# Kernel tuning notes

Measured on AMD Instinct MI355X. Metric: run time of the kernel, lower is better.

## Reference

```python
import jax, jax.numpy as jnp
import numpy as np

# LDPC-like Tanner graph: N variable nodes, M check nodes, dv edges per variable
N_VAR = 8192
N_CHK = 4096
DV = 3
N_EDGE = N_VAR * DV  # 24576 = code.H.E
BATCH = 128
T = 30               # opt.T iterations
EPS = 1e-7


def setup_inputs() -> dict:
    key = jax.random.key(0)
    k1, k2 = jax.random.split(key)
    # channel LLRs for a batch of received codewords, shape (N_VAR, BATCH)
    chn_llr = jax.random.normal(k1, (N_VAR, BATCH), dtype=jnp.float32) * 2.0
    # Tanner graph edge lists: edge e connects variable edge_var[e] <-> check edge_chk[e]
    edge_var = jnp.repeat(jnp.arange(N_VAR, dtype=jnp.int32), DV)
    edge_chk = jax.random.randint(k2, (N_EDGE,), 0, N_CHK, dtype=jnp.int32)
    # gamma_logit = 0  ->  sigmoid = 0.5 = damping_init
    gamma_logit = jnp.zeros((1,), dtype=jnp.float32)
    return {"chn_llr": chn_llr, "gamma_logit": gamma_logit,
            "edge_var": edge_var, "edge_chk": edge_chk}


def reference(chn_llr, gamma_logit, edge_var, edge_chk):
    """T damped sum-product BP iterations over the Tanner graph.

    Returns stacked per-iteration posterior LLRs, shape (T, N_VAR, BATCH).
    """
    gamma = jax.nn.sigmoid(gamma_logit[0])  # damping gate, shared (tie=True)
    segsum = jax.ops.segment_sum

    def step(carry, _):
        msg_C2V, msg_V2C = carry  # each (N_EDGE, BATCH)
        # ---- variable -> check update (extrinsic sum), damped by gamma ----
        var_sum = segsum(msg_C2V, edge_var, num_segments=N_VAR)        # (N_VAR, B)
        v2c_new = chn_llr[edge_var] + var_sum[edge_var] - msg_C2V       # (E, B)
        msg_V2C = gamma * v2c_new + (1.0 - gamma) * msg_V2C
        # ---- check -> variable update (tanh product rule, log/sign domain) ----
        t = jnp.tanh(jnp.clip(msg_V2C, -15.0, 15.0) * 0.5)              # (E, B)
        logabs = jnp.log(jnp.maximum(jnp.abs(t), EPS))
        neg = (t < 0.0).astype(msg_V2C.dtype)
        chk_log = segsum(logabs, edge_chk, num_segments=N_CHK)          # (N_CHK, B)
        chk_neg = segsum(neg, edge_chk, num_segments=N_CHK)
        ext_log = chk_log[edge_chk] - logabs                            # exclude self
        ext_sign = 1.0 - 2.0 * jnp.mod(chk_neg[edge_chk] - neg, 2.0)
        prod = jnp.clip(ext_sign * jnp.exp(ext_log), -1.0 + EPS, 1.0 - EPS)
        msg_C2V = 2.0 * jnp.arctanh(prod)
        # ---- per-iteration posterior LLR output ----
        out = chn_llr + segsum(msg_C2V, edge_var, num_segments=N_VAR)   # (N_VAR, B)
        return (msg_C2V, msg_V2C), out

    init = (jnp.zeros((N_EDGE, BATCH), dtype=chn_llr.dtype),
            jnp.zeros((N_EDGE, BATCH), dtype=chn_llr.dtype))
    _, outputs = jax.lax.scan(step, init, None, length=T)
    return outputs  # (T, N_VAR, BATCH)
```

## Files before the change

kernel.cpp:

```cpp
#include <hip/hip_runtime.h>
#include <math.h>

#define N_VAR 8192
#define N_CHK 4096
#define DV 3
#define N_EDGE (N_VAR * DV)
#define BATCH 128
#define T_ITERS 30
#define ELLW 24
#define SLOT_MAX (N_EDGE + 3 * N_CHK)

#define LOG2E 1.44269504088896340736f
#define LN2   0.69314718055994530942f

typedef _Float16 h4 __attribute__((ext_vector_type(4)));
typedef _Float16 h2 __attribute__((ext_vector_type(2)));

__device__ __forceinline__ float tanh_half(float x) {
    float ex = __builtin_amdgcn_exp2f(x * LOG2E);
    float t = 1.0f - 2.0f * __builtin_amdgcn_rcpf(ex + 1.0f);
    float s = (x < 0.0f) ? -1.0f : 1.0f;
    return s * fmaxf(fabsf(t), 1e-7f);
}

__device__ __forceinline__ float atanh2(float p) {
    const float lim = 1.0f - 1e-7f;
    p = fminf(fmaxf(p, -lim), lim);
    return (__builtin_amdgcn_logf(1.0f + p) -
            __builtin_amdgcn_logf(1.0f - p)) * LN2;
}

__device__ __forceinline__ float rcp_nr(float x) {
    float r = __builtin_amdgcn_rcpf(x);
    return r * (2.0f - x * r);
}


__global__ void k_ell_scatter(const int* __restrict__ edge_chk,
                              int* __restrict__ deg_arr, int* __restrict__ ell_e) {
    int e = blockIdx.x * blockDim.x + threadIdx.x;
    if (e < N_EDGE) {
        int c = edge_chk[e];
        int pos = atomicAdd(&deg_arr[c], 1);
        if (pos < ELLW) ell_e[c * ELLW + pos] = e;
    }
}

__global__ void k_hist(const int* __restrict__ deg_arr, int* __restrict__ hist) {
    int c = blockIdx.x * 256 + threadIdx.x;
    if (c < N_CHK) {
        int d = deg_arr[c]; if (d > ELLW) d = ELLW;
        atomicAdd(&hist[d], 1);
    }
}

__global__ void k_buckets(const int* __restrict__ hist,
                          int* __restrict__ bucket_base,
                          int* __restrict__ slot_off) {
    if (threadIdx.x == 0 && blockIdx.x == 0) {
        int cb = 0, sb = 0;
        for (int d = 0; d <= ELLW; ++d) {
            bucket_base[d] = cb;
            slot_off[d] = sb;
            int pd = (d == 0) ? 0 : ((d + 3) & ~3);
            cb += hist[d];
            sb += hist[d] * pd;
        }
    }
}

__global__ void k_place(const int* __restrict__ deg_arr, int* __restrict__ cursor,
                        const int* __restrict__ bucket_base,
                        const int* __restrict__ slot_off,
                        int* __restrict__ s_desc_g, int* __restrict__ chk_base) {
    int c = blockIdx.x * 256 + threadIdx.x;
    if (c < N_CHK) {
        int d = deg_arr[c]; if (d > ELLW) d = ELLW;
        int pd = (d + 3) & ~3;
        int pos = atomicAdd(&cursor[d], 1);
        int i = bucket_base[d] + pos;
        int base = slot_off[d] + pos * pd;
        s_desc_g[i] = (base << 5) | d;
        chk_base[c] = base;
    }
}

__global__ void k_slotmap2(const int* __restrict__ ell_e,
                           const int* __restrict__ deg_arr,
                           const int* __restrict__ chk_base,
                           int* __restrict__ slot_e) {
    int gid = blockIdx.x * 256 + threadIdx.x;
    if (gid < N_CHK * ELLW) {
        int c = gid / ELLW;
        int j = gid - c * ELLW;
        int d = deg_arr[c]; if (d > ELLW) d = ELLW;
        if (j < d) slot_e[ell_e[gid]] = chk_base[c] + j;
    }
}

__global__ void k_slot4(const int* __restrict__ slot_e, int4* __restrict__ slot4) {
    int v = blockIdx.x * 256 + threadIdx.x;
    if (v < N_VAR) {
        int4 s;
        s.x = slot_e[3 * v + 0];
        s.y = slot_e[3 * v + 1];
        s.z = slot_e[3 * v + 2];
        s.w = 0;
        slot4[v] = s;
    }
}


__global__ __launch_bounds__(1024) void k_bp2(
        const float* __restrict__ chn,
        const float* __restrict__ gamma_logit,
        const int4* __restrict__ slot4,
        const int* __restrict__ s_desc_g,
        _Float16* __restrict__ outT) {
    __shared__ __align__(16) _Float16 msg[SLOT_MAX];
    const int b = blockIdx.x;
    const int tid = threadIdx.x;

    for (int i = tid; i < SLOT_MAX; i += 1024) msg[i] = (_Float16)0.0f;

    const float g = 1.0f / (1.0f + __builtin_amdgcn_exp2f(-gamma_logit[0] * LOG2E));
    const float om = 1.0f - g;
    const float AT1 = atanh2(1.0f);

    float chn_r[8];
    float v2c_r[8][3];
    int4 s4r[8];
    int desc_r[4];
#pragma unroll
    for (int k = 0; k < 8; ++k) {
        int v = tid + k * 1024;
        chn_r[k] = chn[(size_t)v * BATCH + b];
        s4r[k] = slot4[v];
        v2c_r[k][0] = 0.0f; v2c_r[k][1] = 0.0f; v2c_r[k][2] = 0.0f;
    }
#pragma unroll
    for (int m = 0; m < 4; ++m) desc_r[m] = s_desc_g[m * 1024 + tid];
    __syncthreads();

    const size_t SLICE = (size_t)N_VAR * BATCH;

    for (int t = 0; t < T_ITERS; ++t) {
#pragma unroll
        for (int k = 0; k < 8; ++k) {
            int v = tid + k * 1024;
            int4 s4 = s4r[k];
            float c0 = (float)msg[s4.x];
            float c1 = (float)msg[s4.y];
            float c2 = (float)msg[s4.z];
            float post = chn_r[k] + c0 + c1 + c2;
            if (t > 0) {
                __builtin_nontemporal_store((_Float16)post,
                    &outT[(size_t)(t - 1) * SLICE + (size_t)b * N_VAR + v]);
            }
            float vn0 = g * (post - c0) + om * v2c_r[k][0];
            float vn1 = g * (post - c1) + om * v2c_r[k][1];
            float vn2 = g * (post - c2) + om * v2c_r[k][2];
            v2c_r[k][0] = vn0; v2c_r[k][1] = vn1; v2c_r[k][2] = vn2;
            msg[s4.x] = (_Float16)fminf(fmaxf(vn0, -15.0f), 15.0f);
            msg[s4.y] = (_Float16)fminf(fmaxf(vn1, -15.0f), 15.0f);
            msg[s4.z] = (_Float16)fminf(fmaxf(vn2, -15.0f), 15.0f);
        }
        __syncthreads();

#pragma unroll
        for (int m = 0; m < 4; ++m) {
            int desc = desc_r[m];
            int base = desc >> 5;
            int deg = desc & 31;
            if (deg == 1) {
                msg[base] = (_Float16)AT1;
            } else if (deg > 1) {
                int nw = (deg + 3) >> 2;
                h4 raw[6];
#pragma unroll
                for (int w = 0; w < 6; ++w)
                    if (w < nw) raw[w] = *(const h4*)&msg[base + 4 * w];
                float tv[ELLW];
                float P = 1.0f;
#pragma unroll
                for (int j = 0; j < ELLW; ++j)
                    if (j < deg) {
                        tv[j] = tanh_half((float)raw[j >> 2][j & 3]);
                        P *= tv[j];
                    }
#pragma unroll
                for (int w = 0; w < 6; ++w)
                    if (w < nw) {
                        h4 out_w;
#pragma unroll
                        for (int q = 0; q < 4; ++q) {
                            int j = 4 * w + q;
                            float m2 = (j < deg) ? atanh2(P * rcp_nr(tv[j])) : 0.0f;
                            out_w[q] = (_Float16)m2;
                        }
                        *(h4*)&msg[base + 4 * w] = out_w;
                    }
            }
        }
        __syncthreads();
    }

#pragma unroll
    for (int k = 0; k < 8; ++k) {
        int v = tid + k * 1024;
        int4 s4 = s4r[k];
        float post = chn_r[k] + (float)msg[s4.x] + (float)msg[s4.y] +
                     (float)msg[s4.z];
        __builtin_nontemporal_store((_Float16)post,
            &outT[(size_t)(T_ITERS - 1) * SLICE + (size_t)b * N_VAR + v]);
    }
}


__global__ __launch_bounds__(256) void k_transpose(
        const _Float16* __restrict__ src, float* __restrict__ dst) {
    __shared__ float tile[64][33];
    int t = blockIdx.z;
    int v0 = blockIdx.x * 64;
    int b0 = blockIdx.y * 32;
    int lx = threadIdx.x;
    int ly = threadIdx.y;
    const _Float16* s = src + (size_t)t * N_VAR * BATCH;
    float* d = dst + (size_t)t * N_VAR * BATCH;
#pragma unroll
    for (int i = 0; i < 32; i += 8) {
        int bl = ly + i;
        h2 pv = *(const h2*)&s[(size_t)(b0 + bl) * N_VAR + v0 + 2 * lx];
        tile[2 * lx + 0][bl] = (float)pv.x;
        tile[2 * lx + 1][bl] = (float)pv.y;
    }
    __syncthreads();
#pragma unroll
    for (int j = 0; j < 64; j += 8)
        __builtin_nontemporal_store(tile[j + ly][lx],
            &d[(size_t)(v0 + j + ly) * BATCH + b0 + lx]);
}


extern "C" void kernel_launch(void* const* d_in, const int* in_sizes, int n_in,
                              void* d_out, int out_size, void* d_ws, size_t ws_size,
                              hipStream_t stream) {
    const float* chn         = (const float*)d_in[0];
    const float* gamma_logit = (const float*)d_in[1];
    const int* edge_chk      = (const int*)d_in[3];
    float* out = (float*)d_out;

    int4* slot4      = (int4*)d_ws;
    int* slot_e      = (int*)(slot4 + N_VAR);
    int* ell_e       = slot_e + N_EDGE;
    int* deg_arr     = ell_e + (size_t)N_CHK * ELLW;
    int* chk_base    = deg_arr + N_CHK;
    int* s_desc_g    = chk_base + N_CHK;
    int* hist        = s_desc_g + N_CHK;
    int* cursor      = hist + 32;
    int* bucket_base = cursor + 32;
    int* slot_off    = bucket_base + 32;
    size_t table_bytes = (char*)(slot_off + 32) - (char*)d_ws;
    size_t outT_off = (table_bytes + 255) & ~(size_t)255;
    _Float16* outT = (_Float16*)((char*)d_ws + outT_off);

    (void)hipMemsetAsync(deg_arr, 0, N_CHK * sizeof(int), stream);
    (void)hipMemsetAsync(hist, 0, 64 * sizeof(int), stream);

    k_ell_scatter<<<(N_EDGE + 255) / 256, 256, 0, stream>>>(edge_chk, deg_arr,
                                                            ell_e);
    k_hist<<<N_CHK / 256, 256, 0, stream>>>(deg_arr, hist);
    k_buckets<<<1, 64, 0, stream>>>(hist, bucket_base, slot_off);
    k_place<<<N_CHK / 256, 256, 0, stream>>>(deg_arr, cursor, bucket_base,
                                             slot_off, s_desc_g, chk_base);
    k_slotmap2<<<(N_CHK * ELLW + 255) / 256, 256, 0, stream>>>(ell_e, deg_arr,
                                                               chk_base, slot_e);
    k_slot4<<<N_VAR / 256, 256, 0, stream>>>(slot_e, slot4);

    k_bp2<<<BATCH, 1024, 0, stream>>>(chn, gamma_logit, slot4, s_desc_g, outT);

    dim3 tg(N_VAR / 64, BATCH / 32, T_ITERS);
    dim3 tb(32, 8, 1);
    k_transpose<<<tg, tb, 0, stream>>>(outT, out);
}
```

Before: 550.0 us.

## Use prefix/suffix products for check update and fuse setup kernels

The check-node extrinsic product is now built from prefix and suffix running products instead of dividing the total product by each term with a Newton-refined reciprocal. This removes the reciprocal and its refinement, and avoids division by near-zero tanh values, at the cost of an extra suffix pass and more live registers. Separately, the histogram, bucket-offset and placement setup kernels are merged into one single-block kernel that uses shared-memory atomics. This cuts two launches and a memset.

```diff
diff --git a/kernel.cpp b/kernel.cpp
--- a/kernel.cpp
+++ b/kernel.cpp
@@ -30,11 +30,6 @@
             __builtin_amdgcn_logf(1.0f - p)) * LN2;
 }
 
-__device__ __forceinline__ float rcp_nr(float x) {
-    float r = __builtin_amdgcn_rcpf(x);
-    return r * (2.0f - x * r);
-}
-
 
 __global__ void k_ell_scatter(const int* __restrict__ edge_chk,
                               int* __restrict__ deg_arr, int* __restrict__ ell_e) {
@@ -46,40 +41,35 @@
     }
 }
 
-__global__ void k_hist(const int* __restrict__ deg_arr, int* __restrict__ hist) {
-    int c = blockIdx.x * 256 + threadIdx.x;
-    if (c < N_CHK) {
+__global__ __launch_bounds__(1024) void k_sort(
+        const int* __restrict__ deg_arr,
+        int* __restrict__ s_desc_g,
+        int* __restrict__ chk_base) {
+    __shared__ int hist[32], cursor_s[32], bbase[32], soff[32];
+    const int tid = threadIdx.x;
+    if (tid < 32) { hist[tid] = 0; cursor_s[tid] = 0; }
+    __syncthreads();
+    for (int c = tid; c < N_CHK; c += 1024) {
         int d = deg_arr[c]; if (d > ELLW) d = ELLW;
         atomicAdd(&hist[d], 1);
     }
-}
-
-__global__ void k_buckets(const int* __restrict__ hist,
-                          int* __restrict__ bucket_base,
-                          int* __restrict__ slot_off) {
-    if (threadIdx.x == 0 && blockIdx.x == 0) {
+    __syncthreads();
+    if (tid == 0) {
         int cb = 0, sb = 0;
         for (int d = 0; d <= ELLW; ++d) {
-            bucket_base[d] = cb;
-            slot_off[d] = sb;
+            bbase[d] = cb; soff[d] = sb;
             int pd = (d == 0) ? 0 : ((d + 3) & ~3);
             cb += hist[d];
             sb += hist[d] * pd;
         }
     }
-}
-
-__global__ void k_place(const int* __restrict__ deg_arr, int* __restrict__ cursor,
-                        const int* __restrict__ bucket_base,
-                        const int* __restrict__ slot_off,
-                        int* __restrict__ s_desc_g, int* __restrict__ chk_base) {
-    int c = blockIdx.x * 256 + threadIdx.x;
-    if (c < N_CHK) {
+    __syncthreads();
+    for (int c = tid; c < N_CHK; c += 1024) {
         int d = deg_arr[c]; if (d > ELLW) d = ELLW;
         int pd = (d + 3) & ~3;
-        int pos = atomicAdd(&cursor[d], 1);
-        int i = bucket_base[d] + pos;
-        int base = slot_off[d] + pos * pd;
+        int pos = atomicAdd(&cursor_s[d], 1);
+        int i = bbase[d] + pos;
+        int base = soff[d] + pos * pd;
         s_desc_g[i] = (base << 5) | d;
         chk_base[c] = base;
     }
@@ -181,13 +171,15 @@
                 for (int w = 0; w < 6; ++w)
                     if (w < nw) raw[w] = *(const h4*)&msg[base + 4 * w];
                 float tv[ELLW];
-                float P = 1.0f;
 #pragma unroll
                 for (int j = 0; j < ELLW; ++j)
-                    if (j < deg) {
-                        tv[j] = tanh_half((float)raw[j >> 2][j & 3]);
-                        P *= tv[j];
-                    }
+                    if (j < deg) tv[j] = tanh_half((float)raw[j >> 2][j & 3]);
+                float ext[ELLW];
+                float run = 1.0f;
+#pragma unroll
+                for (int j = ELLW - 1; j >= 0; --j)
+                    if (j < deg) { ext[j] = run; run *= tv[j]; }
+                float pfx = 1.0f;
 #pragma unroll
                 for (int w = 0; w < 6; ++w)
                     if (w < nw) {
@@ -195,7 +187,12 @@
 #pragma unroll
                         for (int q = 0; q < 4; ++q) {
                             int j = 4 * w + q;
-                            float m2 = (j < deg) ? atanh2(P * rcp_nr(tv[j])) : 0.0f;
+                            float m2 = 0.0f;
+                            if (j < deg) {
+                                float p = pfx * ext[j];
+                                pfx *= tv[j];
+                                m2 = atanh2(p);
+                            }
                             out_w[q] = (_Float16)m2;
                         }
                         *(h4*)&msg[base + 4 * w] = out_w;
@@ -250,29 +247,21 @@
     const int* edge_chk      = (const int*)d_in[3];
     float* out = (float*)d_out;
 
-    int4* slot4      = (int4*)d_ws;
-    int* slot_e      = (int*)(slot4 + N_VAR);
-    int* ell_e       = slot_e + N_EDGE;
-    int* deg_arr     = ell_e + (size_t)N_CHK * ELLW;
-    int* chk_base    = deg_arr + N_CHK;
-    int* s_desc_g    = chk_base + N_CHK;
-    int* hist        = s_desc_g + N_CHK;
-    int* cursor      = hist + 32;
-    int* bucket_base = cursor + 32;
-    int* slot_off    = bucket_base + 32;
-    size_t table_bytes = (char*)(slot_off + 32) - (char*)d_ws;
+    int4* slot4   = (int4*)d_ws;
+    int* slot_e   = (int*)(slot4 + N_VAR);
+    int* ell_e    = slot_e + N_EDGE;
+    int* deg_arr  = ell_e + (size_t)N_CHK * ELLW;
+    int* chk_base = deg_arr + N_CHK;
+    int* s_desc_g = chk_base + N_CHK;
+    size_t table_bytes = (char*)(s_desc_g + N_CHK) - (char*)d_ws;
     size_t outT_off = (table_bytes + 255) & ~(size_t)255;
     _Float16* outT = (_Float16*)((char*)d_ws + outT_off);
 
     (void)hipMemsetAsync(deg_arr, 0, N_CHK * sizeof(int), stream);
-    (void)hipMemsetAsync(hist, 0, 64 * sizeof(int), stream);
 
     k_ell_scatter<<<(N_EDGE + 255) / 256, 256, 0, stream>>>(edge_chk, deg_arr,
                                                             ell_e);
-    k_hist<<<N_CHK / 256, 256, 0, stream>>>(deg_arr, hist);
-    k_buckets<<<1, 64, 0, stream>>>(hist, bucket_base, slot_off);
-    k_place<<<N_CHK / 256, 256, 0, stream>>>(deg_arr, cursor, bucket_base,
-                                             slot_off, s_desc_g, chk_base);
+    k_sort<<<1, 1024, 0, stream>>>(deg_arr, s_desc_g, chk_base);
     k_slotmap2<<<(N_CHK * ELLW + 255) / 256, 256, 0, stream>>>(ell_e, deg_arr,
                                                                chk_base, slot_e);
     k_slot4<<<N_VAR / 256, 256, 0, stream>>>(slot_e, slot4);
```

Measured after the change: 678.5 us. +23.4%, slower.
